# Kernel optimization log

Hardware: AMD Instinct MI355X
Metric: run time of the kernel (lower is better)

Reference implementation:

```python
import jax, jax.numpy as jnp
import numpy as np

B, L, D_IN = 2, 4096, 512
H, D_K, D_V, D_OUT = 8, 64, 64, 512


def setup_inputs() -> dict:
    key = jax.random.key(0)
    k0, k1, k2, k3, k4 = jax.random.split(key, 5)
    x = jax.random.normal(k0, (B, L, D_IN), dtype=jnp.float32)
    W_q = jax.random.uniform(k1, (H, D_IN, D_K), dtype=jnp.float32)
    W_k = jax.random.uniform(k2, (H, D_IN, D_K), dtype=jnp.float32)
    W_v = jax.random.uniform(k3, (H, D_IN, D_V), dtype=jnp.float32)
    W_o = jax.random.uniform(k4, (H, D_V, D_OUT), dtype=jnp.float32)
    return {"x": x, "W_q": W_q, "W_k": W_k, "W_v": W_v, "W_o": W_o}


def reference(x, W_q, W_k, W_v, W_o):
    # x: (b, l, d_in); projections per head -> (b, h, l, d)
    Q = jnp.einsum('hjk,blj->bhlk', W_q, x)
    K = jnp.einsum('hjk,blj->bhlk', W_k, x)
    V = jnp.einsum('hjv,blj->bhlv', W_v, x)
    # no softmax: pure bilinear attention (Q K^T) V
    scores = jnp.einsum('bhik,bhjk->bhij', Q, K)          # (b, h, l, l)
    values = jnp.einsum('bhqk,bhkv->bhqv', scores, V)     # (b, h, l, d_v)
    return jnp.einsum('hvo,bhlv->blo', W_o, values)       # (b, l, d_out)
```

## Files before the change

kernel.cpp:

```cpp
#include <hip/hip_runtime.h>
#include <cstdint>


#define BDIM 2
#define LDIM 4096
#define DIN 512
#define HDIM 8
#define DK 64
#define DV 64
#define DOUT 512

using bf16_t = __bf16;
typedef __bf16 bf16x8 __attribute__((ext_vector_type(8)));
typedef float floatx4 __attribute__((ext_vector_type(4)));

__device__ __forceinline__ unsigned short f2bf(float f) {
    unsigned int u = __builtin_bit_cast(unsigned int, f);
    u += 0x7FFFu + ((u >> 16) & 1u);
    return (unsigned short)(u >> 16);
}

__device__ __forceinline__ void gld_lds16(const void* g, void* l) {
    __builtin_amdgcn_global_load_lds(
        (const __attribute__((address_space(1))) void*)g,
        (__attribute__((address_space(3))) void*)l, 16, 0, 0);
}

template <int BM, int BN, int BK, bool TRANS_OUT, int OUT_MODE>
__device__ __forceinline__ void gemm_core(const bf16_t* A, const bf16_t* B,
                                          void* Cp, int K, int lda, int ldb,
                                          int ldc, int tm, int tn) {
    constexpr int WM = BM / 2, WN = BN / 2;
    constexpr int FM = WM / 16, FN = WN / 16;
    constexpr int CPR = BK / 8;
    __shared__ __align__(16) bf16_t As[BM * BK];
    __shared__ __align__(16) bf16_t Bs[BN * BK];
    const int tid = threadIdx.x;
    const int lane = tid & 63;
    const int wr = (tid >> 7) & 1;
    const int wc = (tid >> 6) & 1;

    A += (size_t)tm * lda;
    B += (size_t)tn * ldb;

    floatx4 acc[FM][FN] = {};

    for (int k0 = 0; k0 < K; k0 += BK) {
#pragma unroll
        for (int i = 0; i < (BM * CPR) / 256; ++i) {
            int c = i * 256 + tid;
            int m = c / CPR, kc = c % CPR;
            gld_lds16(A + (size_t)m * lda + k0 + kc * 8, As + c * 8);
        }
#pragma unroll
        for (int i = 0; i < (BN * CPR) / 256; ++i) {
            int c = i * 256 + tid;
            int m = c / CPR, kc = c % CPR;
            gld_lds16(B + (size_t)m * ldb + k0 + kc * 8, Bs + c * 8);
        }
        __syncthreads();

#pragma unroll
        for (int kk = 0; kk < BK; kk += 32) {
            bf16x8 aF[FM], bF[FN];
#pragma unroll
            for (int fm = 0; fm < FM; ++fm)
                aF[fm] = *(const bf16x8*)(As + (wr * WM + fm * 16 + (lane & 15)) * BK +
                                          kk + (lane >> 4) * 8);
#pragma unroll
            for (int fn = 0; fn < FN; ++fn)
                bF[fn] = *(const bf16x8*)(Bs + (wc * WN + fn * 16 + (lane & 15)) * BK +
                                          kk + (lane >> 4) * 8);
#pragma unroll
            for (int fm = 0; fm < FM; ++fm)
#pragma unroll
                for (int fn = 0; fn < FN; ++fn)
                    acc[fm][fn] = __builtin_amdgcn_mfma_f32_16x16x32_bf16(
                        aF[fm], bF[fn], acc[fm][fn], 0, 0, 0);
        }
        __syncthreads();
    }

    const int cr4 = (lane >> 4) * 4;
    const int cn = lane & 15;
#pragma unroll
    for (int fm = 0; fm < FM; ++fm)
#pragma unroll
        for (int fn = 0; fn < FN; ++fn)
#pragma unroll
            for (int r = 0; r < 4; ++r) {
                int m = tm + wr * WM + fm * 16 + cr4 + r;
                int n = tn + wc * WN + fn * 16 + cn;
                size_t idx = TRANS_OUT ? ((size_t)n * ldc + m)
                                       : ((size_t)m * ldc + n);
                if (OUT_MODE == 0)
                    ((float*)Cp)[idx] = acc[fm][fn][r];
                else if (OUT_MODE == 1)
                    ((unsigned short*)Cp)[idx] = f2bf(acc[fm][fn][r]);
                else
                    atomicAdd((float*)Cp + idx, acc[fm][fn][r]);
            }
}

__global__ __launch_bounds__(256) void k_xtx(const bf16_t* xT, float* G32) {
    const int t = blockIdx.x;
    const int chunk = blockIdx.y;
    const int b = blockIdx.z;
    const int i0 = (t >> 3) * 128, j0 = (t & 7) * 64;
    const bf16_t* Xb = xT + (size_t)b * DIN * LDIM + (size_t)chunk * 512;
    gemm_core<128, 64, 64, false, 2>(Xb, Xb, G32 + (size_t)b * DIN * DIN, 512,
                                     LDIM, LDIM, DIN, i0, j0);
}

__global__ __launch_bounds__(256) void k_gv(const bf16_t* WkT, const float* G32,
                                            unsigned short* T2) {
    const int jt = blockIdx.x, h = blockIdx.y, b = blockIdx.z;
    const int j0 = jt * 64;
    __shared__ __align__(16) bf16_t As[64 * 64];
    __shared__ __align__(16) bf16_t Bs[64 * 64];
    const int tid = threadIdx.x;
    const int lane = tid & 63;
    const int wr = (tid >> 7) & 1, wc = (tid >> 6) & 1;
    const int cr4 = (lane >> 4) * 4, cn = lane & 15;

    const bf16_t* A = WkT + (size_t)h * DK * DIN;
    const float* Gb = G32 + (size_t)b * DIN * DIN + (size_t)j0 * DIN;

    floatx4 acc[2][2] = {};
    for (int k0 = 0; k0 < DIN; k0 += 64) {
#pragma unroll
        for (int i = 0; i < 2; ++i) {
            int c = i * 256 + tid, m = c >> 3, kc = c & 7;
            gld_lds16(A + (size_t)m * DIN + k0 + kc * 8, As + c * 8);
        }
#pragma unroll
        for (int i = 0; i < 2; ++i) {
            int c = i * 256 + tid, n = c >> 3, kc = c & 7;
            const float* src = Gb + (size_t)n * DIN + k0 + kc * 8;
            float4 v0 = *(const float4*)src;
            float4 v1 = *(const float4*)(src + 4);
            unsigned short o[8] = {f2bf(v0.x), f2bf(v0.y), f2bf(v0.z), f2bf(v0.w),
                                   f2bf(v1.x), f2bf(v1.y), f2bf(v1.z), f2bf(v1.w)};
            *(uint4*)((unsigned short*)Bs + (size_t)c * 8) = *(const uint4*)o;
        }
        __syncthreads();
#pragma unroll
        for (int kk = 0; kk < 64; kk += 32) {
            bf16x8 aF[2], bF[2];
#pragma unroll
            for (int f = 0; f < 2; ++f) {
                aF[f] = *(const bf16x8*)(As + (wr * 32 + f * 16 + cn) * 64 + kk +
                                         (lane >> 4) * 8);
                bF[f] = *(const bf16x8*)(Bs + (wc * 32 + f * 16 + cn) * 64 + kk +
                                         (lane >> 4) * 8);
            }
#pragma unroll
            for (int fm = 0; fm < 2; ++fm)
#pragma unroll
                for (int fn = 0; fn < 2; ++fn)
                    acc[fm][fn] = __builtin_amdgcn_mfma_f32_16x16x32_bf16(
                        aF[fm], bF[fn], acc[fm][fn], 0, 0, 0);
        }
        __syncthreads();
    }

    unsigned short* dst = T2 + (size_t)(b * HDIM + h) * DK * DIN;
#pragma unroll
    for (int fm = 0; fm < 2; ++fm)
#pragma unroll
        for (int fn = 0; fn < 2; ++fn)
#pragma unroll
            for (int r = 0; r < 4; ++r) {
                int m = wr * 32 + fm * 16 + cr4 + r;
                int n = wc * 32 + fn * 16 + cn;
                dst[(size_t)m * DIN + j0 + n] = f2bf(acc[fm][fn][r]);
            }
}

__global__ __launch_bounds__(256) void k_m(const bf16_t* T2, const bf16_t* WvT,
                                           float* M32) {
    const int h = blockIdx.x, b = blockIdx.y;
    gemm_core<64, 64, 64, false, 0>(T2 + (size_t)(b * HDIM + h) * DK * DIN,
                                    WvT + (size_t)h * DV * DIN,
                                    M32 + (size_t)(b * HDIM + h) * (DK * DV),
                                    DIN, DIN, DIN, DV, 0, 0);
}

__global__ __launch_bounds__(256) void k_tail(const bf16_t* WqC, const bf16_t* WoT,
                                              const float* M32, unsigned short* CT) {
    int i0 = blockIdx.x * 64, o0 = blockIdx.y * 64, b = blockIdx.z;
    __shared__ __align__(16) bf16_t Aq[64 * 64];
    __shared__ __align__(16) bf16_t Ws[64 * 64];
    __shared__ __align__(16) bf16_t Msh[64 * 64];
    __shared__ __align__(16) bf16_t PTs[64 * 64];
    const int tid = threadIdx.x;
    const int lane = tid & 63;
    const int wr = (tid >> 7) & 1, wc = (tid >> 6) & 1;
    const int cr4 = (lane >> 4) * 4, cn = lane & 15;

    floatx4 acc[2][2] = {};

    for (int h = 0; h < HDIM; ++h) {
#pragma unroll
        for (int i = 0; i < 2; ++i) {
            int c = i * 256 + tid, m = c >> 3, kc = c & 7;
            gld_lds16(WqC + (size_t)(i0 + m) * DIN + h * 64 + kc * 8, Aq + c * 8);
            gld_lds16(WoT + ((size_t)h * DOUT + o0 + m) * DV + kc * 8, Ws + c * 8);
        }
        const float* Mh = M32 + ((size_t)(b * HDIM + h)) * (DK * DV);
#pragma unroll
        for (int i = 0; i < 4; ++i) {
            int idx = (i * 256 + tid) * 4;
            float4 v = *(const float4*)(Mh + idx);
            *(ushort4*)((unsigned short*)Msh + idx) =
                make_ushort4(f2bf(v.x), f2bf(v.y), f2bf(v.z), f2bf(v.w));
        }
        __syncthreads();

        floatx4 pt[2][2] = {};
#pragma unroll
        for (int kk = 0; kk < 64; kk += 32) {
            bf16x8 aF[2], bF[2];
#pragma unroll
            for (int f = 0; f < 2; ++f) {
                aF[f] = *(const bf16x8*)(Ws + (wr * 32 + f * 16 + cn) * 64 + kk +
                                         (lane >> 4) * 8);
                bF[f] = *(const bf16x8*)(Msh + (wc * 32 + f * 16 + cn) * 64 + kk +
                                         (lane >> 4) * 8);
            }
#pragma unroll
            for (int fm = 0; fm < 2; ++fm)
#pragma unroll
                for (int fn = 0; fn < 2; ++fn)
                    pt[fm][fn] = __builtin_amdgcn_mfma_f32_16x16x32_bf16(
                        aF[fm], bF[fn], pt[fm][fn], 0, 0, 0);
        }
#pragma unroll
        for (int fm = 0; fm < 2; ++fm)
#pragma unroll
            for (int fn = 0; fn < 2; ++fn)
#pragma unroll
                for (int r = 0; r < 4; ++r) {
                    int m = wr * 32 + fm * 16 + cr4 + r;
                    int n = wc * 32 + fn * 16 + cn;
                    ((unsigned short*)PTs)[m * 64 + n] = f2bf(pt[fm][fn][r]);
                }
        __syncthreads();

#pragma unroll
        for (int kk = 0; kk < 64; kk += 32) {
            bf16x8 aF[2], bF[2];
#pragma unroll
            for (int f = 0; f < 2; ++f) {
                aF[f] = *(const bf16x8*)(PTs + (wr * 32 + f * 16 + cn) * 64 + kk +
                                         (lane >> 4) * 8);
                bF[f] = *(const bf16x8*)(Aq + (wc * 32 + f * 16 + cn) * 64 + kk +
                                         (lane >> 4) * 8);
            }
#pragma unroll
            for (int fm = 0; fm < 2; ++fm)
#pragma unroll
                for (int fn = 0; fn < 2; ++fn)
                    acc[fm][fn] = __builtin_amdgcn_mfma_f32_16x16x32_bf16(
                        aF[fm], bF[fn], acc[fm][fn], 0, 0, 0);
        }
        __syncthreads();
    }

    unsigned short* CTb = CT + (size_t)b * DIN * DOUT;
#pragma unroll
    for (int fm = 0; fm < 2; ++fm)
#pragma unroll
        for (int fn = 0; fn < 2; ++fn)
#pragma unroll
            for (int r = 0; r < 4; ++r) {
                int m = wr * 32 + fm * 16 + cr4 + r;
                int n = wc * 32 + fn * 16 + cn;
                CTb[(size_t)(o0 + m) * DIN + i0 + n] = f2bf(acc[fm][fn][r]);
            }
}

__global__ __launch_bounds__(256) void k_out(const bf16_t* x16, const bf16_t* CT,
                                             float* out) {
    int b = blockIdx.z;
    gemm_core<64, 128, 64, false, 0>(x16 + (size_t)b * LDIM * DIN,
                                     CT + (size_t)b * DIN * DOUT,
                                     out + (size_t)b * LDIM * DOUT, DIN, DIN,
                                     DIN, DOUT, blockIdx.x * 64,
                                     blockIdx.y * 128);
}

__global__ __launch_bounds__(256) void k_prep3(
    const float* x, const float* Wq, const float* Wk, const float* Wv,
    const float* Wo, unsigned short* xb, unsigned short* xT,
    unsigned short* WqC, unsigned short* WkT, unsigned short* WvT,
    unsigned short* WoT, float* G32) {
    __shared__ unsigned short T[64][65];
    int tr = threadIdx.x >> 4, tc4 = (threadIdx.x & 15) * 4;
    int bid = blockIdx.x;
    if (bid < 2048) {
        size_t base = ((size_t)bid * 256 + threadIdx.x) * 8;
        float4 v0 = *(const float4*)(x + base);
        float4 v1 = *(const float4*)(x + base + 4);
        unsigned short o[8] = {f2bf(v0.x), f2bf(v0.y), f2bf(v0.z), f2bf(v0.w),
                               f2bf(v1.x), f2bf(v1.y), f2bf(v1.z), f2bf(v1.w)};
        *(uint4*)(xb + base) = *(const uint4*)o;
        return;
    }
    if (bid < 3072) {
        int p_ = bid - 2048;
        int b = p_ >> 9;
        int q = p_ & 511;
        int lt = q >> 3, it = q & 7;
        const float* src = x + (size_t)b * LDIM * DIN + (size_t)lt * 64 * DIN +
                           (size_t)it * 64;
        unsigned short* dst = xT + (size_t)b * DIN * LDIM +
                              (size_t)it * 64 * LDIM + (size_t)lt * 64;
#pragma unroll
        for (int p = 0; p < 4; ++p) {
            int r = p * 16 + tr;
            float4 v = *(const float4*)(src + (size_t)r * DIN + tc4);
            T[r][tc4 + 0] = f2bf(v.x); T[r][tc4 + 1] = f2bf(v.y);
            T[r][tc4 + 2] = f2bf(v.z); T[r][tc4 + 3] = f2bf(v.w);
        }
        __syncthreads();
#pragma unroll
        for (int p = 0; p < 4; ++p) {
            int c = p * 16 + tr;
            ushort4 u = make_ushort4(T[tc4 + 0][c], T[tc4 + 1][c], T[tc4 + 2][c],
                                     T[tc4 + 3][c]);
            *(ushort4*)(dst + (size_t)c * LDIM + tc4) = u;
        }
        return;
    }
    if (bid >= 3328) {
        size_t g = ((size_t)(bid - 3328) * 256 + threadIdx.x) * 32;
        float4 z4 = make_float4(0.f, 0.f, 0.f, 0.f);
#pragma unroll
        for (int q = 0; q < 8; ++q) *(float4*)(G32 + g + q * 4) = z4;
        return;
    }
    int p_ = bid - 3072;
    int t = p_ & 7, job = (p_ >> 3) & 3, h = p_ >> 5;
    if (job == 0) {
        const float* src = Wq + (size_t)h * DIN * DK;
#pragma unroll
        for (int p = 0; p < 4; ++p) {
            int i = t * 64 + p * 16 + tr;
            float4 v = *(const float4*)(src + (size_t)i * DK + tc4);
            *(ushort4*)(WqC + (size_t)i * (HDIM * DK) + h * DK + tc4) =
                make_ushort4(f2bf(v.x), f2bf(v.y), f2bf(v.z), f2bf(v.w));
        }
        return;
    }
    const float* src;
    unsigned short* dst;
    int rows, cols, r0, c0;
    if (job == 1) {
        src = Wk + (size_t)h * DIN * DK;
        dst = WkT + (size_t)h * DK * DIN;
        rows = DIN; cols = DK; r0 = t * 64; c0 = 0;
    } else if (job == 2) {
        src = Wv + (size_t)h * DIN * DV;
        dst = WvT + (size_t)h * DV * DIN;
        rows = DIN; cols = DV; r0 = t * 64; c0 = 0;
    } else {
        src = Wo + (size_t)h * DV * DOUT;
        dst = WoT + (size_t)h * DOUT * DV;
        rows = DV; cols = DOUT; r0 = 0; c0 = t * 64;
    }
#pragma unroll
    for (int p = 0; p < 4; ++p) {
        int r = p * 16 + tr;
        float4 v = *(const float4*)(src + (size_t)(r0 + r) * cols + c0 + tc4);
        T[r][tc4 + 0] = f2bf(v.x); T[r][tc4 + 1] = f2bf(v.y);
        T[r][tc4 + 2] = f2bf(v.z); T[r][tc4 + 3] = f2bf(v.w);
    }
    __syncthreads();
#pragma unroll
    for (int p = 0; p < 4; ++p) {
        int c = p * 16 + tr;
        ushort4 u = make_ushort4(T[tc4 + 0][c], T[tc4 + 1][c], T[tc4 + 2][c],
                                 T[tc4 + 3][c]);
        *(ushort4*)(dst + (size_t)(c0 + c) * rows + r0 + tc4) = u;
    }
}

extern "C" void kernel_launch(void* const* d_in, const int* in_sizes, int n_in,
                              void* d_out, int out_size, void* d_ws, size_t ws_size,
                              hipStream_t stream) {
    const float* x  = (const float*)d_in[0];
    const float* Wq = (const float*)d_in[1];
    const float* Wk = (const float*)d_in[2];
    const float* Wv = (const float*)d_in[3];
    const float* Wo = (const float*)d_in[4];
    float* out = (float*)d_out;

    unsigned short* w = (unsigned short*)d_ws;
    unsigned short* xb16 = w; w += (size_t)BDIM * LDIM * DIN;
    unsigned short* xT16 = w; w += (size_t)BDIM * DIN * LDIM;
    unsigned short* WqC  = w; w += (size_t)DIN * HDIM * DK;
    unsigned short* WkT  = w; w += (size_t)HDIM * DK * DIN;
    unsigned short* WvT  = w; w += (size_t)HDIM * DV * DIN;
    unsigned short* WoT  = w; w += (size_t)HDIM * DOUT * DV;
    unsigned short* CT   = w; w += (size_t)BDIM * DIN * DOUT;
    unsigned short* T2   = w; w += (size_t)BDIM * HDIM * DK * DIN;
    float* G32 = (float*)(((uintptr_t)w + 255) & ~(uintptr_t)255);
    float* M32 = G32 + (size_t)BDIM * DIN * DIN;

    k_prep3<<<dim3(3392), 256, 0, stream>>>(x, Wq, Wk, Wv, Wo, xb16, xT16,
                                            WqC, WkT, WvT, WoT, G32);
    k_xtx<<<dim3(32, 8, BDIM), 256, 0, stream>>>((const bf16_t*)xT16, G32);
    k_gv<<<dim3(8, HDIM, BDIM), 256, 0, stream>>>((const bf16_t*)WkT, G32, T2);
    k_m<<<dim3(HDIM, BDIM), 256, 0, stream>>>((const bf16_t*)T2,
                                              (const bf16_t*)WvT, M32);
    k_tail<<<dim3(8, 8, BDIM), 256, 0, stream>>>((const bf16_t*)WqC,
                                                 (const bf16_t*)WoT, M32, CT);
    k_out<<<dim3(LDIM / 64, DOUT / 128, BDIM), 256, 0, stream>>>(
        (const bf16_t*)xb16, (const bf16_t*)CT, out);
}
```

Before: 145.8 us.

## Split-K Gram into chunk partials, fuse G·Wk·Wv stages, merge x casts

The x^T x Gram kernel now writes four per-chunk fp32 partial results instead of atomically accumulating eight chunks into one buffer. The partials are summed when the next stage loads them. The G·Wk and T2·Wv stages are fused into one kernel that keeps the T2 tile in LDS and atomically accumulates M, which removes the T2 round trip and a launch. The prep kernel writes the row-major and transposed bf16 copies of x in one pass, and zeroes M instead of G. The cost is a larger workspace, four times the reads of G in the fused kernel, and fewer blocks in the Gram kernel.

```diff
diff --git a/kernel.cpp b/kernel.cpp
--- a/kernel.cpp
+++ b/kernel.cpp
@@ -9,6 +9,7 @@
 #define DK 64
 #define DV 64
 #define DOUT 512
+#define NCHUNK 4
 
 using bf16_t = __bf16;
 typedef __bf16 bf16x8 __attribute__((ext_vector_type(8)));
@@ -95,36 +96,36 @@
                                        : ((size_t)m * ldc + n);
                 if (OUT_MODE == 0)
                     ((float*)Cp)[idx] = acc[fm][fn][r];
-                else if (OUT_MODE == 1)
+                else
                     ((unsigned short*)Cp)[idx] = f2bf(acc[fm][fn][r]);
-                else
-                    atomicAdd((float*)Cp + idx, acc[fm][fn][r]);
-            }
-}
-
-__global__ __launch_bounds__(256) void k_xtx(const bf16_t* xT, float* G32) {
+            }
+}
+
+__global__ __launch_bounds__(256) void k_xtx(const bf16_t* xT, float* Gp) {
     const int t = blockIdx.x;
     const int chunk = blockIdx.y;
     const int b = blockIdx.z;
     const int i0 = (t >> 3) * 128, j0 = (t & 7) * 64;
-    const bf16_t* Xb = xT + (size_t)b * DIN * LDIM + (size_t)chunk * 512;
-    gemm_core<128, 64, 64, false, 2>(Xb, Xb, G32 + (size_t)b * DIN * DIN, 512,
-                                     LDIM, LDIM, DIN, i0, j0);
-}
-
-__global__ __launch_bounds__(256) void k_gv(const bf16_t* WkT, const float* G32,
-                                            unsigned short* T2) {
+    const bf16_t* Xb = xT + (size_t)b * DIN * LDIM + (size_t)chunk * 1024;
+    float* Gc = Gp + ((size_t)chunk * BDIM + b) * DIN * DIN;
+    gemm_core<128, 64, 64, false, 0>(Xb, Xb, Gc, 1024, LDIM, LDIM, DIN, i0, j0);
+}
+
+__global__ __launch_bounds__(256) void k_gvm(const bf16_t* WkT, const bf16_t* WvT,
+                                             const float* Gp, float* M32) {
     const int jt = blockIdx.x, h = blockIdx.y, b = blockIdx.z;
     const int j0 = jt * 64;
     __shared__ __align__(16) bf16_t As[64 * 64];
     __shared__ __align__(16) bf16_t Bs[64 * 64];
+    __shared__ __align__(16) bf16_t Vs[64 * 64];
+    __shared__ __align__(16) bf16_t T2s[64 * 64];
     const int tid = threadIdx.x;
     const int lane = tid & 63;
     const int wr = (tid >> 7) & 1, wc = (tid >> 6) & 1;
     const int cr4 = (lane >> 4) * 4, cn = lane & 15;
 
     const bf16_t* A = WkT + (size_t)h * DK * DIN;
-    const float* Gb = G32 + (size_t)b * DIN * DIN + (size_t)j0 * DIN;
+    constexpr size_t GSTRIDE = (size_t)BDIM * DIN * DIN;
 
     floatx4 acc[2][2] = {};
     for (int k0 = 0; k0 < DIN; k0 += 64) {
@@ -136,11 +137,19 @@
 #pragma unroll
         for (int i = 0; i < 2; ++i) {
             int c = i * 256 + tid, n = c >> 3, kc = c & 7;
-            const float* src = Gb + (size_t)n * DIN + k0 + kc * 8;
-            float4 v0 = *(const float4*)src;
-            float4 v1 = *(const float4*)(src + 4);
-            unsigned short o[8] = {f2bf(v0.x), f2bf(v0.y), f2bf(v0.z), f2bf(v0.w),
-                                   f2bf(v1.x), f2bf(v1.y), f2bf(v1.z), f2bf(v1.w)};
+            const float* g0 = Gp + ((size_t)b * DIN + j0 + n) * DIN + k0 + kc * 8;
+            float4 s0 = *(const float4*)g0;
+            float4 s1 = *(const float4*)(g0 + 4);
+#pragma unroll
+            for (int ch = 1; ch < NCHUNK; ++ch) {
+                const float* gc = g0 + (size_t)ch * GSTRIDE;
+                float4 t0 = *(const float4*)gc;
+                float4 t1 = *(const float4*)(gc + 4);
+                s0.x += t0.x; s0.y += t0.y; s0.z += t0.z; s0.w += t0.w;
+                s1.x += t1.x; s1.y += t1.y; s1.z += t1.z; s1.w += t1.w;
+            }
+            unsigned short o[8] = {f2bf(s0.x), f2bf(s0.y), f2bf(s0.z), f2bf(s0.w),
+                                   f2bf(s1.x), f2bf(s1.y), f2bf(s1.z), f2bf(s1.w)};
             *(uint4*)((unsigned short*)Bs + (size_t)c * 8) = *(const uint4*)o;
         }
         __syncthreads();
@@ -164,7 +173,6 @@
         __syncthreads();
     }
 
-    unsigned short* dst = T2 + (size_t)(b * HDIM + h) * DK * DIN;
 #pragma unroll
     for (int fm = 0; fm < 2; ++fm)
 #pragma unroll
@@ -173,17 +181,44 @@
             for (int r = 0; r < 4; ++r) {
                 int m = wr * 32 + fm * 16 + cr4 + r;
                 int n = wc * 32 + fn * 16 + cn;
-                dst[(size_t)m * DIN + j0 + n] = f2bf(acc[fm][fn][r]);
-            }
-}
-
-__global__ __launch_bounds__(256) void k_m(const bf16_t* T2, const bf16_t* WvT,
-                                           float* M32) {
-    const int h = blockIdx.x, b = blockIdx.y;
-    gemm_core<64, 64, 64, false, 0>(T2 + (size_t)(b * HDIM + h) * DK * DIN,
-                                    WvT + (size_t)h * DV * DIN,
-                                    M32 + (size_t)(b * HDIM + h) * (DK * DV),
-                                    DIN, DIN, DIN, DV, 0, 0);
+                ((unsigned short*)T2s)[m * 64 + n] = f2bf(acc[fm][fn][r]);
+            }
+#pragma unroll
+    for (int i = 0; i < 2; ++i) {
+        int c = i * 256 + tid, v = c >> 3, kc = c & 7;
+        gld_lds16(WvT + ((size_t)h * DV + v) * DIN + j0 + kc * 8, Vs + c * 8);
+    }
+    __syncthreads();
+
+    floatx4 mm[2][2] = {};
+#pragma unroll
+    for (int kk = 0; kk < 64; kk += 32) {
+        bf16x8 aF[2], bF[2];
+#pragma unroll
+        for (int f = 0; f < 2; ++f) {
+            aF[f] = *(const bf16x8*)(T2s + (wr * 32 + f * 16 + cn) * 64 + kk +
+                                     (lane >> 4) * 8);
+            bF[f] = *(const bf16x8*)(Vs + (wc * 32 + f * 16 + cn) * 64 + kk +
+                                     (lane >> 4) * 8);
+        }
+#pragma unroll
+        for (int fm = 0; fm < 2; ++fm)
+#pragma unroll
+            for (int fn = 0; fn < 2; ++fn)
+                mm[fm][fn] = __builtin_amdgcn_mfma_f32_16x16x32_bf16(
+                    aF[fm], bF[fn], mm[fm][fn], 0, 0, 0);
+    }
+    float* Mh = M32 + ((size_t)(b * HDIM + h)) * (DK * DV);
+#pragma unroll
+    for (int fm = 0; fm < 2; ++fm)
+#pragma unroll
+        for (int fn = 0; fn < 2; ++fn)
+#pragma unroll
+            for (int r = 0; r < 4; ++r) {
+                int dk = wr * 32 + fm * 16 + cr4 + r;
+                int v = wc * 32 + fn * 16 + cn;
+                atomicAdd(&Mh[dk * 64 + v], mm[fm][fn][r]);
+            }
 }
 
 __global__ __launch_bounds__(256) void k_tail(const bf16_t* WqC, const bf16_t* WoT,
@@ -290,38 +325,32 @@
                                      blockIdx.y * 128);
 }
 
-__global__ __launch_bounds__(256) void k_prep3(
+__global__ __launch_bounds__(256) void k_prep4(
     const float* x, const float* Wq, const float* Wk, const float* Wv,
     const float* Wo, unsigned short* xb, unsigned short* xT,
     unsigned short* WqC, unsigned short* WkT, unsigned short* WvT,
-    unsigned short* WoT, float* G32) {
+    unsigned short* WoT, float* M32) {
     __shared__ unsigned short T[64][65];
     int tr = threadIdx.x >> 4, tc4 = (threadIdx.x & 15) * 4;
     int bid = blockIdx.x;
-    if (bid < 2048) {
-        size_t base = ((size_t)bid * 256 + threadIdx.x) * 8;
-        float4 v0 = *(const float4*)(x + base);
-        float4 v1 = *(const float4*)(x + base + 4);
-        unsigned short o[8] = {f2bf(v0.x), f2bf(v0.y), f2bf(v0.z), f2bf(v0.w),
-                               f2bf(v1.x), f2bf(v1.y), f2bf(v1.z), f2bf(v1.w)};
-        *(uint4*)(xb + base) = *(const uint4*)o;
-        return;
-    }
-    if (bid < 3072) {
-        int p_ = bid - 2048;
-        int b = p_ >> 9;
-        int q = p_ & 511;
+    if (bid < 1024) {
+        int b = bid >> 9;
+        int q = bid & 511;
         int lt = q >> 3, it = q & 7;
         const float* src = x + (size_t)b * LDIM * DIN + (size_t)lt * 64 * DIN +
                            (size_t)it * 64;
-        unsigned short* dst = xT + (size_t)b * DIN * LDIM +
-                              (size_t)it * 64 * LDIM + (size_t)lt * 64;
+        unsigned short* d0 = xb + (size_t)b * LDIM * DIN + (size_t)lt * 64 * DIN +
+                             (size_t)it * 64;
+        unsigned short* d1 = xT + (size_t)b * DIN * LDIM + (size_t)it * 64 * LDIM +
+                             (size_t)lt * 64;
 #pragma unroll
         for (int p = 0; p < 4; ++p) {
             int r = p * 16 + tr;
             float4 v = *(const float4*)(src + (size_t)r * DIN + tc4);
-            T[r][tc4 + 0] = f2bf(v.x); T[r][tc4 + 1] = f2bf(v.y);
-            T[r][tc4 + 2] = f2bf(v.z); T[r][tc4 + 3] = f2bf(v.w);
+            ushort4 u = make_ushort4(f2bf(v.x), f2bf(v.y), f2bf(v.z), f2bf(v.w));
+            *(ushort4*)(d0 + (size_t)r * DIN + tc4) = u;
+            T[r][tc4 + 0] = u.x; T[r][tc4 + 1] = u.y;
+            T[r][tc4 + 2] = u.z; T[r][tc4 + 3] = u.w;
         }
         __syncthreads();
 #pragma unroll
@@ -329,18 +358,18 @@
             int c = p * 16 + tr;
             ushort4 u = make_ushort4(T[tc4 + 0][c], T[tc4 + 1][c], T[tc4 + 2][c],
                                      T[tc4 + 3][c]);
-            *(ushort4*)(dst + (size_t)c * LDIM + tc4) = u;
+            *(ushort4*)(d1 + (size_t)c * LDIM + tc4) = u;
         }
         return;
     }
-    if (bid >= 3328) {
-        size_t g = ((size_t)(bid - 3328) * 256 + threadIdx.x) * 32;
+    if (bid >= 1280) {
+        size_t g = ((size_t)(bid - 1280) * 256 + threadIdx.x) * 32;
         float4 z4 = make_float4(0.f, 0.f, 0.f, 0.f);
 #pragma unroll
-        for (int q = 0; q < 8; ++q) *(float4*)(G32 + g + q * 4) = z4;
+        for (int q = 0; q < 8; ++q) *(float4*)(M32 + g + q * 4) = z4;
         return;
     }
-    int p_ = bid - 3072;
+    int p_ = bid - 1024;
     int t = p_ & 7, job = (p_ >> 3) & 3, h = p_ >> 5;
     if (job == 0) {
         const float* src = Wq + (size_t)h * DIN * DK;
@@ -404,16 +433,14 @@
     unsigned short* WvT  = w; w += (size_t)HDIM * DV * DIN;
     unsigned short* WoT  = w; w += (size_t)HDIM * DOUT * DV;
     unsigned short* CT   = w; w += (size_t)BDIM * DIN * DOUT;
-    unsigned short* T2   = w; w += (size_t)BDIM * HDIM * DK * DIN;
-    float* G32 = (float*)(((uintptr_t)w + 255) & ~(uintptr_t)255);
-    float* M32 = G32 + (size_t)BDIM * DIN * DIN;
-
-    k_prep3<<<dim3(3392), 256, 0, stream>>>(x, Wq, Wk, Wv, Wo, xb16, xT16,
-                                            WqC, WkT, WvT, WoT, G32);
-    k_xtx<<<dim3(32, 8, BDIM), 256, 0, stream>>>((const bf16_t*)xT16, G32);
-    k_gv<<<dim3(8, HDIM, BDIM), 256, 0, stream>>>((const bf16_t*)WkT, G32, T2);
-    k_m<<<dim3(HDIM, BDIM), 256, 0, stream>>>((const bf16_t*)T2,
-                                              (const bf16_t*)WvT, M32);
+    float* Gp = (float*)(((uintptr_t)w + 255) & ~(uintptr_t)255);
+    float* M32 = Gp + (size_t)NCHUNK * BDIM * DIN * DIN;
+
+    k_prep4<<<dim3(1288), 256, 0, stream>>>(x, Wq, Wk, Wv, Wo, xb16, xT16,
+                                            WqC, WkT, WvT, WoT, M32);
+    k_xtx<<<dim3(32, NCHUNK, BDIM), 256, 0, stream>>>((const bf16_t*)xT16, Gp);
+    k_gvm<<<dim3(8, HDIM, BDIM), 256, 0, stream>>>((const bf16_t*)WkT,
+                                                   (const bf16_t*)WvT, Gp, M32);
     k_tail<<<dim3(8, 8, BDIM), 256, 0, stream>>>((const bf16_t*)WqC,
                                                  (const bf16_t*)WoT, M32, CT);
     k_out<<<dim3(LDIM / 64, DOUT / 128, BDIM), 256, 0, stream>>>(
```

After: 135.5 us. 1.08x faster.
